# Kernel tuning notes

Measured on AMD Instinct MI355X. Metric: run time of the kernel, lower is better.

## Reference

```python
import jax, jax.numpy as jnp
import numpy as np

FIELD_DIMS = [1000, 50000, 20000, 10000, 5000, 2000, 1000, 500, 100000, 8000,
              4000, 2000, 1000, 500, 250, 100, 50, 30, 20, 10, 5, 3, 2]
F = len(FIELD_DIMS)           # num_fields = 23
V = sum(FIELD_DIMS)           # total vocab = 205470
D = 16                        # embed_dim
B = 4096                      # batch
OFFSETS = jnp.asarray(np.array((0, *np.cumsum(FIELD_DIMS)[:-1]), dtype=np.int64))


def setup_inputs() -> dict:
    key = jax.random.key(0)
    k_e, k_w, k_x = jax.random.split(key, 3)
    # per-field indices in each field's valid range
    xkeys = jax.random.split(k_x, F)
    x = jnp.stack([jax.random.randint(xkeys[i], (B,), 0, FIELD_DIMS[i])
                   for i in range(F)], axis=1).astype(jnp.int64)  # [B, F]
    # F field-aware embedding tables stacked: [F, V, D] (xavier-ish scale)
    E = jax.random.normal(k_e, (F, V, D), dtype=jnp.float32) * 0.01
    # linear term weights (nn.Embedding(V, 1)) and bias
    W_lin = jax.random.normal(k_w, (V, 1), dtype=jnp.float32) * 0.01
    bias = jnp.zeros((1,), dtype=jnp.float32)
    return {"x": x, "E": E, "W_lin": W_lin, "bias": bias}


def reference(x, E, W_lin, bias):
    idx = x + OFFSETS[None, :]                       # [B, F] global indices
    # A[b, i, j, d] = embedding-table i looked up at field j's index
    A = jnp.transpose(jnp.take(E, idx, axis=1), (1, 0, 2, 3))  # [B, F, F, D]
    # pairwise FFM term: sum_{i<j} sum_d A[b,i,j,d] * A[b,j,i,d]
    P = A * jnp.swapaxes(A, 1, 2)                    # [B, F, F, D]
    mask = jnp.triu(jnp.ones((F, F), dtype=A.dtype), k=1)
    ffm = jnp.einsum('bijd,ij->b', P, mask)          # [B]
    # linear term: sum over fields of per-index scalar weight, plus bias
    linear = jnp.sum(jnp.take(W_lin, idx, axis=0), axis=1) + bias  # [B, 1]
    return jax.nn.sigmoid(linear[:, 0] + ffm)        # [B]
```

## Files before the change

### kernel.cpp

```cpp
#include <hip/hip_runtime.h>
#include <cstdint>

#define NF 23
#define ED 16
static const long long VTOT = 205470;
#define NPAIR 253

__constant__ int OFFSETS_D[NF] = {
    0, 1000, 51000, 71000, 81000, 86000, 88000, 89000, 89500, 189500,
    197500, 201500, 203500, 204500, 205000, 205250, 205350, 205400,
    205430, 205450, 205460, 205465, 205468
};

struct PairTab { unsigned char pi[256]; unsigned char pj[256]; };
static constexpr PairTab make_pairs() {
    PairTab t{};
    int p = 0;
    for (int i = 0; i < NF; ++i)
        for (int j = i + 1; j < NF; ++j) { t.pi[p] = (unsigned char)i; t.pj[p] = (unsigned char)j; ++p; }
    for (; p < 256; ++p) { t.pi[p] = 0; t.pj[p] = 1; }
    return t;
}
__constant__ PairTab PAIRS = make_pairs();

__global__ __launch_bounds__(256) void ffm_kernel(
    const int* __restrict__ x,
    const float* __restrict__ E,
    const float* __restrict__ W,
    const float* __restrict__ bias,
    float* __restrict__ out,
    int B)
{
    __shared__ int s_idx[4][NF];

    const int lane = threadIdx.x & 63;
    const int wid  = threadIdx.x >> 6;
    const int b    = blockIdx.x * 4 + wid;
    const bool valid_b = (b < B);

    float acc = 0.0f;

    if (valid_b && lane < NF) {
        int ix = x[(long long)b * NF + lane] + OFFSETS_D[lane];
        s_idx[wid][lane] = ix;
        acc = W[ix];
    }
    __syncthreads();

    if (valid_b) {
        const int grp = lane >> 2;
        const int dq  = lane & 3;

        #pragma unroll 4
        for (int it = 0; it < 16; ++it) {
            const int p = it * 16 + grp;
            if (p < NPAIR) {
                const int i = PAIRS.pi[p];
                const int j = PAIRS.pj[p];
                const long long idx_i = s_idx[wid][i];
                const long long idx_j = s_idx[wid][j];
                const float4 a = *reinterpret_cast<const float4*>(
                    E + ((long long)i * VTOT + idx_j) * ED + dq * 4);
                const float4 c = *reinterpret_cast<const float4*>(
                    E + ((long long)j * VTOT + idx_i) * ED + dq * 4);
                acc += a.x * c.x + a.y * c.y + a.z * c.z + a.w * c.w;
            }
        }
    }

    #pragma unroll
    for (int off = 32; off; off >>= 1) acc += __shfl_xor(acc, off, 64);

    if (valid_b && lane == 0) {
        const float z = acc + bias[0];
        out[b] = 1.0f / (1.0f + __expf(-z));
    }
}

extern "C" void kernel_launch(void* const* d_in, const int* in_sizes, int n_in,
                              void* d_out, int out_size, void* d_ws, size_t ws_size,
                              hipStream_t stream) {
    const int*   x    = (const int*)d_in[0];
    const float* E    = (const float*)d_in[1];
    const float* W    = (const float*)d_in[2];
    const float* bias = (const float*)d_in[3];
    float* out = (float*)d_out;

    const int B = in_sizes[0] / NF;
    const int blocks = (B + 3) / 4;
    ffm_kernel<<<blocks, 256, 0, stream>>>(x, E, W, bias, out, B);
}
```

Measured before the change: 357.2 us.

## Assign one batch row per block and batch all gathers before reducing

Each 256-thread block now handles a single batch row, with its four wavefronts splitting the 253 field pairs so each thread issues at most four pairs of float4 gathers up front. The per-wave results are combined through shared memory. Offsets are computed in 32-bit unsigned arithmetic, which fits the table size. The aim is more memory-level parallelism per thread and more blocks in flight to hide random gather latency, at the cost of an extra barrier, a shared-memory reduction and about four times as many blocks.

```diff
diff --git a/kernel.cpp b/kernel.cpp
--- a/kernel.cpp
+++ b/kernel.cpp
@@ -3,7 +3,7 @@
 
 #define NF 23
 #define ED 16
-static const long long VTOT = 205470;
+#define VTOT 205470
 #define NPAIR 253
 
 __constant__ int OFFSETS_D[NF] = {
@@ -28,51 +28,57 @@
     const float* __restrict__ E,
     const float* __restrict__ W,
     const float* __restrict__ bias,
-    float* __restrict__ out,
-    int B)
+    float* __restrict__ out)
 {
-    __shared__ int s_idx[4][NF];
+    __shared__ int   s_idx[NF];
+    __shared__ float s_part[4];
 
-    const int lane = threadIdx.x & 63;
-    const int wid  = threadIdx.x >> 6;
-    const int b    = blockIdx.x * 4 + wid;
-    const bool valid_b = (b < B);
+    const int tid  = threadIdx.x;
+    const int lane = tid & 63;
+    const int wid  = tid >> 6;
+    const int b    = blockIdx.x;
 
     float acc = 0.0f;
 
-    if (valid_b && lane < NF) {
-        int ix = x[(long long)b * NF + lane] + OFFSETS_D[lane];
-        s_idx[wid][lane] = ix;
+    if (tid < NF) {
+        const int ix = x[b * NF + tid] + OFFSETS_D[tid];
+        s_idx[tid] = ix;
         acc = W[ix];
     }
     __syncthreads();
 
-    if (valid_b) {
-        const int grp = lane >> 2;
-        const int dq  = lane & 3;
+    const int grp = lane >> 2;
+    const int dq  = lane & 3;
 
-        #pragma unroll 4
-        for (int it = 0; it < 16; ++it) {
-            const int p = it * 16 + grp;
-            if (p < NPAIR) {
-                const int i = PAIRS.pi[p];
-                const int j = PAIRS.pj[p];
-                const long long idx_i = s_idx[wid][i];
-                const long long idx_j = s_idx[wid][j];
-                const float4 a = *reinterpret_cast<const float4*>(
-                    E + ((long long)i * VTOT + idx_j) * ED + dq * 4);
-                const float4 c = *reinterpret_cast<const float4*>(
-                    E + ((long long)j * VTOT + idx_i) * ED + dq * 4);
-                acc += a.x * c.x + a.y * c.y + a.z * c.z + a.w * c.w;
-            }
-        }
+    float4 av[4], cv[4];
+    bool   vld[4];
+    #pragma unroll
+    for (int it = 0; it < 4; ++it) {
+        const int p  = wid * 64 + it * 16 + grp;
+        vld[it] = (p < NPAIR);
+        const int ps = vld[it] ? p : 0;
+        const int i  = PAIRS.pi[ps];
+        const int j  = PAIRS.pj[ps];
+        const unsigned off_a = (unsigned)(i * VTOT + s_idx[j]) * ED + dq * 4;
+        const unsigned off_c = (unsigned)(j * VTOT + s_idx[i]) * ED + dq * 4;
+        av[it] = *reinterpret_cast<const float4*>(E + off_a);
+        cv[it] = *reinterpret_cast<const float4*>(E + off_c);
+    }
+
+    #pragma unroll
+    for (int it = 0; it < 4; ++it) {
+        const float m = vld[it] ? 1.0f : 0.0f;
+        acc += m * (av[it].x * cv[it].x + av[it].y * cv[it].y +
+                    av[it].z * cv[it].z + av[it].w * cv[it].w);
     }
 
     #pragma unroll
     for (int off = 32; off; off >>= 1) acc += __shfl_xor(acc, off, 64);
+    if (lane == 0) s_part[wid] = acc;
+    __syncthreads();
 
-    if (valid_b && lane == 0) {
-        const float z = acc + bias[0];
+    if (tid == 0) {
+        const float z = s_part[0] + s_part[1] + s_part[2] + s_part[3] + bias[0];
         out[b] = 1.0f / (1.0f + __expf(-z));
     }
 }
@@ -87,6 +93,5 @@
     float* out = (float*)d_out;
 
     const int B = in_sizes[0] / NF;
-    const int blocks = (B + 3) / 4;
-    ffm_kernel<<<blocks, 256, 0, stream>>>(x, E, W, bias, out, B);
+    ffm_kernel<<<B, 256, 0, stream>>>(x, E, W, bias, out);
 }
```

Result: no change. 357.9 us (+0.2%).
